# Optimization experiments

Hardware: AMD Instinct MI355X
Metric: run time of the kernel (lower is better)

## Reference

```python
import jax, jax.numpy as jnp
import numpy as np


def setup_inputs() -> dict:
    key = jax.random.key(0)
    kq, kk, kv = jax.random.split(key, 3)
    B, T, D = 8, 4096, 64
    q = jax.random.normal(kq, (B, T, D), dtype=jnp.float32)
    k = jax.random.normal(kk, (B, T, D), dtype=jnp.float32)
    v = jax.random.normal(kv, (B, T, D), dtype=jnp.float32)
    return {"q": q, "k": k, "v": v}


def reference(q, k, v):
    # q,k,v: [b, t, d]
    b, t_q, d = q.shape
    t_k = k.shape[1]
    scale = 1.0 / jnp.sqrt(jnp.asarray(d, dtype=q.dtype))
    qk = jnp.einsum('bqd,bkd->bqk', q, k) * scale  # [b, t_q, t_k]
    # causal mask: positions t2 > t1 set to -inf (replaces the Python double-loop)
    causal_mask = jnp.arange(t_k)[None, :] > jnp.arange(t_q)[:, None]  # [t_q, t_k]
    qk = jnp.where(causal_mask[None, :, :], -jnp.inf, qk)
    attn = jax.nn.softmax(qk, axis=-1)
    return jnp.einsum('bqk,bkd->bqd', attn, v)
```

## Files before the change

### kernel.cpp

```cpp
#include <hip/hip_runtime.h>

namespace {

constexpr float QSC = 0.18033688f;

typedef short bf16x8 __attribute__((ext_vector_type(8)));
typedef float f32x4 __attribute__((ext_vector_type(4)));

typedef __attribute__((address_space(3))) unsigned int lds_u32;
typedef __attribute__((address_space(1))) const unsigned int gbl_u32;

__device__ inline float exp2x(float x) { return __builtin_amdgcn_exp2f(x); }

__device__ inline unsigned int pack2(float a, float b) {
  unsigned int ua = __builtin_bit_cast(unsigned int, a);
  unsigned int ub = __builtin_bit_cast(unsigned int, b);
  ua = (ua + 0x8000u) >> 16;
  ub = (ub + 0x8000u) & 0xFFFF0000u;
  return ua | ub;
}

__device__ inline void gl_lds16(const unsigned short* g, unsigned short* l) {
  __builtin_amdgcn_global_load_lds((gbl_u32*)g, (lds_u32*)l, 16, 0, 0);
}

__device__ inline bf16x8 ld16(const unsigned short* p) {
  uint4 u = *(const uint4*)p;
  return __builtin_bit_cast(bf16x8, u);
}

__device__ inline void pswap32(unsigned int& a, unsigned int& b) {
  asm volatile("v_permlane32_swap_b32 %0, %1" : "+v"(a), "+v"(b));
}
__device__ inline void pswap16(unsigned int& a, unsigned int& b) {
  asm volatile("v_permlane16_swap_b32 %0, %1" : "+v"(a), "+v"(b));
}

__global__ __launch_bounds__(256) void prep(const float* __restrict__ K,
                                            const float* __restrict__ V,
                                            unsigned short* __restrict__ Kbf,
                                            unsigned short* __restrict__ Vtb) {
  __shared__ float Vl[64 * 65];
  const int bid = blockIdx.x;
  const int b = bid >> 6, kt = bid & 63;
  const int tid = threadIdx.x;
  const float4* Ks4 = (const float4*)(K + ((size_t)b * 4096 + kt * 64) * 64);
  const float4* Vs4 = (const float4*)(V + ((size_t)b * 4096 + kt * 64) * 64);
  #pragma unroll
  for (int i = 0; i < 4; ++i) {
    int idx = tid + 256 * i;
    int row = idx >> 4, c4 = idx & 15;
    float4 t = Ks4[idx];
    *(uint2*)&Kbf[((size_t)b * 4096 + kt * 64 + row) * 64 + c4 * 4] =
        make_uint2(pack2(t.x, t.y), pack2(t.z, t.w));
    float4 tv = Vs4[idx];
    float* d = &Vl[row * 65 + c4 * 4];
    d[0] = tv.x; d[1] = tv.y; d[2] = tv.z; d[3] = tv.w;
  }
  __syncthreads();
  #pragma unroll
  for (int i = 0; i < 4; ++i) {
    int idx = tid + 256 * i;
    int dd = idx >> 4, kc = idx & 15;
    float a  = Vl[(kc * 4 + 0) * 65 + dd];
    float b2 = Vl[(kc * 4 + 1) * 65 + dd];
    float c  = Vl[(kc * 4 + 2) * 65 + dd];
    float e  = Vl[(kc * 4 + 3) * 65 + dd];
    *(uint2*)&Vtb[((size_t)b * 64 + dd) * 4096 + kt * 64 + kc * 4] =
        make_uint2(pack2(a, b2), pack2(c, e));
  }
}

template <int NS>
__launch_bounds__(256, 5)
__global__ void fa_mfma(const float* __restrict__ Q,
                        float* __restrict__ O,
                        const unsigned short* __restrict__ Kbf,
                        const unsigned short* __restrict__ Vtb,
                        float* __restrict__ Opart,
                        float* __restrict__ lsum) {
  __shared__ __align__(16) unsigned short smem[16384];

  const int bid = blockIdx.x;
  const int qt = 63 - bid / (8 * NS);
  const int b  = (bid / NS) & 7;
  const int s  = bid % NS;

  const int tid  = threadIdx.x;
  const int wg   = tid >> 6;
  const int lane = tid & 63;
  const int quad = lane >> 4;
  const int lc   = lane & 15;

  unsigned short* Kb0 = smem;
  unsigned short* Kb1 = smem + 4096;
  unsigned short* Vb0 = smem + 8192;
  unsigned short* Vb1 = smem + 12288;

  const unsigned short* Kt_g = Kbf + (size_t)b * 4096 * 64;
  const unsigned short* Vt_g = Vtb + (size_t)b * 64 * 4096;

  const int r0 = wg * 16 + (lane >> 3);
  const int c0 = (lane & 7) ^ (r0 & 7);

  const int ph0 = (quad ^ (lc & 7)) * 8;
  const int ph1 = ((4 + quad) ^ (lc & 7)) * 8;

  const size_t tile_off = ((size_t)b * 4096 + (size_t)qt * 64) * 64;
  const float* Qb = Q + tile_off;

  const int nIter = (qt >= s) ? ((qt - s) / NS + 1) : 0;

  {
    const int kt0 = (s <= qt) ? s : qt;
    gl_lds16(Kt_g + (size_t)(kt0 * 64 + r0) * 64 + c0 * 8, Kb0 + wg * 1024);
    gl_lds16(Kt_g + (size_t)(kt0 * 64 + r0 + 8) * 64 + c0 * 8, Kb0 + wg * 1024 + 512);
    gl_lds16(Vt_g + (size_t)r0 * 4096 + kt0 * 64 + c0 * 8, Vb0 + wg * 1024);
    gl_lds16(Vt_g + (size_t)(r0 + 8) * 4096 + kt0 * 64 + c0 * 8, Vb0 + wg * 1024 + 512);
  }

  bf16x8 qf[2];
  {
    const float* qrow = Qb + (wg * 16 + lc) * 64 + quad * 8;
    #pragma unroll
    for (int ks = 0; ks < 2; ++ks) {
      float4 x = *(const float4*)(qrow + ks * 32);
      float4 y = *(const float4*)(qrow + ks * 32 + 4);
      uint4 u = make_uint4(pack2(x.x * QSC, x.y * QSC), pack2(x.z * QSC, x.w * QSC),
                           pack2(y.x * QSC, y.y * QSC), pack2(y.z * QSC, y.w * QSC));
      qf[ks] = __builtin_bit_cast(bf16x8, u);
    }
  }

  float l_i = 0.0f;
  f32x4 o[4];
  #pragma unroll
  for (int nt = 0; nt < 4; ++nt) o[nt] = f32x4{0.f, 0.f, 0.f, 0.f};

  const int qrow = wg * 16 + lc;

  auto body = [&](const unsigned short* Kcur, const unsigned short* Vcur, bool diag) __attribute__((always_inline)) {
    f32x4 st[4];
    __builtin_amdgcn_s_setprio(1);
    #pragma unroll
    for (int t = 0; t < 4; ++t) {
      f32x4 c = {0.f, 0.f, 0.f, 0.f};
      c = __builtin_amdgcn_mfma_f32_16x16x32_bf16(ld16(&Kcur[(t * 16 + lc) * 64 + ph0]), qf[0], c, 0, 0, 0);
      c = __builtin_amdgcn_mfma_f32_16x16x32_bf16(ld16(&Kcur[(t * 16 + lc) * 64 + ph1]), qf[1], c, 0, 0, 0);
      st[t] = c;
    }
    __builtin_amdgcn_s_setprio(0);

    unsigned int pc[4][2];
    #pragma unroll
    for (int t = 0; t < 4; ++t) {
      float e[4];
      #pragma unroll
      for (int r = 0; r < 4; ++r) {
        float v = st[t][r];
        if (diag) {
          int key_l = 16 * t + quad * 4 + r;
          if (key_l > qrow) v = -1e30f;
        }
        e[r] = exp2x(v);
      }
      l_i += (e[0] + e[1]) + (e[2] + e[3]);
      pc[t][0] = pack2(e[0], e[1]);
      pc[t][1] = pack2(e[2], e[3]);
    }

    __builtin_amdgcn_s_setprio(1);
    #pragma unroll
    for (int ks = 0; ks < 2; ++ks) {
      unsigned int x0 = pc[2 * ks][0], y0 = pc[2 * ks + 1][0];
      unsigned int x1 = pc[2 * ks][1], y1 = pc[2 * ks + 1][1];
      pswap32(x0, y0); pswap16(x0, y0);
      pswap32(x1, y1); pswap16(x1, y1);
      bf16x8 a = __builtin_bit_cast(bf16x8, make_uint4(x0, x1, y0, y1));
      const int ph = ks ? ph1 : ph0;
      #pragma unroll
      for (int nt = 0; nt < 4; ++nt) {
        o[nt] = __builtin_amdgcn_mfma_f32_16x16x32_bf16(a, ld16(&Vcur[(nt * 16 + lc) * 64 + ph]), o[nt], 0, 0, 0);
      }
    }
    __builtin_amdgcn_s_setprio(0);
  };

  for (int i = 0; i + 1 < nIter; ++i) {
    const unsigned short* Kcur = (i & 1) ? Kb1 : Kb0;
    const unsigned short* Vcur = (i & 1) ? Vb1 : Vb0;
    unsigned short* Knxt = (i & 1) ? Kb0 : Kb1;
    unsigned short* Vnxt = (i & 1) ? Vb0 : Vb1;

    asm volatile("s_waitcnt vmcnt(0)" ::: "memory");
    __builtin_amdgcn_s_barrier();

    const int ktn = NS * (i + 1) + s;
    const unsigned short* gk = Kt_g + (size_t)(ktn * 64) * 64;
    gl_lds16(gk + (size_t)r0 * 64 + c0 * 8, Knxt + wg * 1024);
    gl_lds16(gk + (size_t)(r0 + 8) * 64 + c0 * 8, Knxt + wg * 1024 + 512);
    const unsigned short* gv = Vt_g + ktn * 64;
    gl_lds16(gv + (size_t)r0 * 4096 + c0 * 8, Vnxt + wg * 1024);
    gl_lds16(gv + (size_t)(r0 + 8) * 4096 + c0 * 8, Vnxt + wg * 1024 + 512);

    body(Kcur, Vcur, false);
  }

  if (nIter > 0) {
    const int il = nIter - 1;
    const unsigned short* Kcur = (il & 1) ? Kb1 : Kb0;
    const unsigned short* Vcur = (il & 1) ? Vb1 : Vb0;
    asm volatile("s_waitcnt vmcnt(0)" ::: "memory");
    __builtin_amdgcn_s_barrier();
    body(Kcur, Vcur, (NS * il + s) == qt);
  }

  l_i += __shfl_xor(l_i, 16);
  l_i += __shfl_xor(l_i, 32);

  if constexpr (NS == 1) {
    float linv = 1.0f / l_i;
    float lv[4];
    #pragma unroll
    for (int r = 0; r < 4; ++r) lv[r] = __shfl(linv, quad * 4 + r);
    float* Ob = O + tile_off;
    #pragma unroll
    for (int r = 0; r < 4; ++r) {
      int row = wg * 16 + quad * 4 + r;
      #pragma unroll
      for (int nt = 0; nt < 4; ++nt)
        Ob[row * 64 + nt * 16 + lc] = o[nt][r] * lv[r];
    }
  } else {
    float* Oslot = (s == 0) ? (O + tile_off)
                            : (Opart + (size_t)(s - 1) * 2097152 + tile_off);
    #pragma unroll
    for (int r = 0; r < 4; ++r) {
      int row = wg * 16 + quad * 4 + r;
      #pragma unroll
      for (int nt = 0; nt < 4; ++nt)
        Oslot[row * 64 + nt * 16 + lc] = o[nt][r];
    }
    if (quad == 0)
      lsum[s * 32768 + b * 4096 + qt * 64 + wg * 16 + lc] = l_i;
  }
}

template <int NS>
__global__ __launch_bounds__(256) void fa_merge(float* __restrict__ O,
                                               const float* __restrict__ Opart,
                                               const float* __restrict__ lsum) {
  const int f = (blockIdx.x * 256 + threadIdx.x) * 4;
  const int row = f >> 6;
  float l = lsum[row];
  float4 acc = *(const float4*)&O[f];
  #pragma unroll
  for (int s2 = 1; s2 < NS; ++s2) {
    l += lsum[s2 * 32768 + row];
    float4 p = *(const float4*)&Opart[(size_t)(s2 - 1) * 2097152 + f];
    acc.x += p.x; acc.y += p.y; acc.z += p.z; acc.w += p.w;
  }
  const float linv = 1.0f / l;
  acc.x *= linv; acc.y *= linv; acc.z *= linv; acc.w *= linv;
  *(float4*)&O[f] = acc;
}

}

extern "C" void kernel_launch(void* const* d_in, const int* in_sizes, int n_in,
                              void* d_out, int out_size, void* d_ws, size_t ws_size,
                              hipStream_t stream) {
  const float* q = (const float*)d_in[0];
  const float* k = (const float*)d_in[1];
  const float* v = (const float*)d_in[2];
  float* out = (float*)d_out;

  unsigned short* Kbf = (unsigned short*)d_ws;
  unsigned short* Vtb = Kbf + (size_t)8 * 4096 * 64;
  float* Opart = (float*)(Vtb + (size_t)8 * 4096 * 64);
  auto need = [&](int ns) {
    return (size_t)16 * 1024 * 1024 / 2 +
           (size_t)(ns - 1) * 2097152 * 4 +
           (size_t)ns * 32768 * 4;
  };

  prep<<<dim3(512), dim3(256), 0, stream>>>(k, v, Kbf, Vtb);

  if (ws_size >= need(4)) {
    float* lsum = Opart + (size_t)3 * 2097152;
    fa_mfma<4><<<dim3(2048), dim3(256), 0, stream>>>(q, out, Kbf, Vtb, Opart, lsum);
    fa_merge<4><<<dim3(2048), dim3(256), 0, stream>>>(out, Opart, lsum);
  } else if (ws_size >= need(2)) {
    float* lsum = Opart + (size_t)1 * 2097152;
    fa_mfma<2><<<dim3(1024), dim3(256), 0, stream>>>(q, out, Kbf, Vtb, Opart, lsum);
    fa_merge<2><<<dim3(2048), dim3(256), 0, stream>>>(out, Opart, lsum);
  } else {
    fa_mfma<1><<<dim3(512), dim3(256), 0, stream>>>(q, out, Kbf, Vtb, nullptr, nullptr);
  }
}
```

Baseline: 108.8 us.

## Split attention tile 2x2 across waves by query and key halves, reduce via LDS

Each wave now handles 32 queries against 32 keys of the 64-key tile instead of 16 queries against all 64 keys. K and V fragments are loaded into registers once and reused across two query subtiles, which cuts LDS reads per MFMA. Partial outputs and row sums from the two key-half waves are combined through shared memory at the end. The change also switches bf16 packing to the hardware v_cvt_pk_bf16_f32 instruction and lowers the occupancy hint from 5 to 4 waves to allow more registers. The cost is extra registers for the doubled accumulators, plus an LDS reduction and barrier in the epilogue.

New measurement: 109.8 us. No clear change (+0.9%).

```diff
diff --git a/kernel.cpp b/kernel.cpp
--- a/kernel.cpp
+++ b/kernel.cpp
@@ -18,6 +18,12 @@
   ua = (ua + 0x8000u) >> 16;
   ub = (ub + 0x8000u) & 0xFFFF0000u;
   return ua | ub;
+}
+
+__device__ inline unsigned int cvtpk(float a, float b) {
+  unsigned int r;
+  asm("v_cvt_pk_bf16_f32 %0, %1, %2" : "=v"(r) : "v"(a), "v"(b));
+  return r;
 }
 
 __device__ inline void gl_lds16(const unsigned short* g, unsigned short* l) {
@@ -72,7 +78,7 @@
 }
 
 template <int NS>
-__launch_bounds__(256, 5)
+__launch_bounds__(256, 4)
 __global__ void fa_mfma(const float* __restrict__ Q,
                         float* __restrict__ O,
                         const unsigned short* __restrict__ Kbf,
@@ -87,7 +93,9 @@
   const int s  = bid % NS;
 
   const int tid  = threadIdx.x;
-  const int wg   = tid >> 6;
+  const int w    = tid >> 6;
+  const int kh   = w & 1;
+  const int qh   = w >> 1;
   const int lane = tid & 63;
   const int quad = lane >> 4;
   const int lc   = lane & 15;
@@ -100,11 +108,12 @@
   const unsigned short* Kt_g = Kbf + (size_t)b * 4096 * 64;
   const unsigned short* Vt_g = Vtb + (size_t)b * 64 * 4096;
 
-  const int r0 = wg * 16 + (lane >> 3);
+  const int r0 = w * 16 + (lane >> 3);
   const int c0 = (lane & 7) ^ (r0 & 7);
 
   const int ph0 = (quad ^ (lc & 7)) * 8;
   const int ph1 = ((4 + quad) ^ (lc & 7)) * 8;
+  const int phv = ((kh * 4 + quad) ^ (lc & 7)) * 8;
 
   const size_t tile_off = ((size_t)b * 4096 + (size_t)qt * 64) * 64;
   const float* Qb = Q + tile_off;
@@ -113,75 +122,89 @@
 
   {
     const int kt0 = (s <= qt) ? s : qt;
-    gl_lds16(Kt_g + (size_t)(kt0 * 64 + r0) * 64 + c0 * 8, Kb0 + wg * 1024);
-    gl_lds16(Kt_g + (size_t)(kt0 * 64 + r0 + 8) * 64 + c0 * 8, Kb0 + wg * 1024 + 512);
-    gl_lds16(Vt_g + (size_t)r0 * 4096 + kt0 * 64 + c0 * 8, Vb0 + wg * 1024);
-    gl_lds16(Vt_g + (size_t)(r0 + 8) * 4096 + kt0 * 64 + c0 * 8, Vb0 + wg * 1024 + 512);
-  }
-
-  bf16x8 qf[2];
-  {
-    const float* qrow = Qb + (wg * 16 + lc) * 64 + quad * 8;
+    gl_lds16(Kt_g + (size_t)(kt0 * 64 + r0) * 64 + c0 * 8, Kb0 + w * 1024);
+    gl_lds16(Kt_g + (size_t)(kt0 * 64 + r0 + 8) * 64 + c0 * 8, Kb0 + w * 1024 + 512);
+    gl_lds16(Vt_g + (size_t)r0 * 4096 + kt0 * 64 + c0 * 8, Vb0 + w * 1024);
+    gl_lds16(Vt_g + (size_t)(r0 + 8) * 4096 + kt0 * 64 + c0 * 8, Vb0 + w * 1024 + 512);
+  }
+
+  bf16x8 qf[2][2];
+  #pragma unroll
+  for (int tq = 0; tq < 2; ++tq) {
+    const float* qrow = Qb + (qh * 32 + tq * 16 + lc) * 64 + quad * 8;
     #pragma unroll
     for (int ks = 0; ks < 2; ++ks) {
       float4 x = *(const float4*)(qrow + ks * 32);
       float4 y = *(const float4*)(qrow + ks * 32 + 4);
       uint4 u = make_uint4(pack2(x.x * QSC, x.y * QSC), pack2(x.z * QSC, x.w * QSC),
                            pack2(y.x * QSC, y.y * QSC), pack2(y.z * QSC, y.w * QSC));
-      qf[ks] = __builtin_bit_cast(bf16x8, u);
-    }
-  }
-
-  float l_i = 0.0f;
-  f32x4 o[4];
-  #pragma unroll
-  for (int nt = 0; nt < 4; ++nt) o[nt] = f32x4{0.f, 0.f, 0.f, 0.f};
-
-  const int qrow = wg * 16 + lc;
+      qf[tq][ks] = __builtin_bit_cast(bf16x8, u);
+    }
+  }
+
+  float l4[2] = {0.0f, 0.0f};
+  f32x4 o[2][4];
+  #pragma unroll
+  for (int tq = 0; tq < 2; ++tq)
+    #pragma unroll
+    for (int td = 0; td < 4; ++td) o[tq][td] = f32x4{0.f, 0.f, 0.f, 0.f};
 
   auto body = [&](const unsigned short* Kcur, const unsigned short* Vcur, bool diag) __attribute__((always_inline)) {
-    f32x4 st[4];
+    bf16x8 kf[2][2];
+    #pragma unroll
+    for (int tk = 0; tk < 2; ++tk) {
+      kf[tk][0] = ld16(&Kcur[(kh * 32 + tk * 16 + lc) * 64 + ph0]);
+      kf[tk][1] = ld16(&Kcur[(kh * 32 + tk * 16 + lc) * 64 + ph1]);
+    }
+    f32x4 st[2][2];
     __builtin_amdgcn_s_setprio(1);
     #pragma unroll
-    for (int t = 0; t < 4; ++t) {
-      f32x4 c = {0.f, 0.f, 0.f, 0.f};
-      c = __builtin_amdgcn_mfma_f32_16x16x32_bf16(ld16(&Kcur[(t * 16 + lc) * 64 + ph0]), qf[0], c, 0, 0, 0);
-      c = __builtin_amdgcn_mfma_f32_16x16x32_bf16(ld16(&Kcur[(t * 16 + lc) * 64 + ph1]), qf[1], c, 0, 0, 0);
-      st[t] = c;
-    }
+    for (int tk = 0; tk < 2; ++tk)
+      #pragma unroll
+      for (int tq = 0; tq < 2; ++tq) {
+        f32x4 c = {0.f, 0.f, 0.f, 0.f};
+        c = __builtin_amdgcn_mfma_f32_16x16x32_bf16(kf[tk][0], qf[tq][0], c, 0, 0, 0);
+        c = __builtin_amdgcn_mfma_f32_16x16x32_bf16(kf[tk][1], qf[tq][1], c, 0, 0, 0);
+        st[tk][tq] = c;
+      }
     __builtin_amdgcn_s_setprio(0);
 
-    unsigned int pc[4][2];
-    #pragma unroll
-    for (int t = 0; t < 4; ++t) {
-      float e[4];
-      #pragma unroll
-      for (int r = 0; r < 4; ++r) {
-        float v = st[t][r];
-        if (diag) {
-          int key_l = 16 * t + quad * 4 + r;
-          if (key_l > qrow) v = -1e30f;
+    unsigned int pc[2][2][2];
+    #pragma unroll
+    for (int tk = 0; tk < 2; ++tk)
+      #pragma unroll
+      for (int tq = 0; tq < 2; ++tq) {
+        float e[4];
+        #pragma unroll
+        for (int r = 0; r < 4; ++r) {
+          float v = st[tk][tq][r];
+          if (diag) {
+            int key_l = kh * 32 + tk * 16 + quad * 4 + r;
+            int q_l   = qh * 32 + tq * 16 + lc;
+            if (key_l > q_l) v = -1e30f;
+          }
+          e[r] = exp2x(v);
         }
-        e[r] = exp2x(v);
-      }
-      l_i += (e[0] + e[1]) + (e[2] + e[3]);
-      pc[t][0] = pack2(e[0], e[1]);
-      pc[t][1] = pack2(e[2], e[3]);
-    }
-
+        l4[tq] += (e[0] + e[1]) + (e[2] + e[3]);
+        pc[tk][tq][0] = cvtpk(e[0], e[1]);
+        pc[tk][tq][1] = cvtpk(e[2], e[3]);
+      }
+
+    bf16x8 vf[4];
+    #pragma unroll
+    for (int td = 0; td < 4; ++td)
+      vf[td] = ld16(&Vcur[(td * 16 + lc) * 64 + phv]);
     __builtin_amdgcn_s_setprio(1);
     #pragma unroll
-    for (int ks = 0; ks < 2; ++ks) {
-      unsigned int x0 = pc[2 * ks][0], y0 = pc[2 * ks + 1][0];
-      unsigned int x1 = pc[2 * ks][1], y1 = pc[2 * ks + 1][1];
+    for (int tq = 0; tq < 2; ++tq) {
+      unsigned int x0 = pc[0][tq][0], y0 = pc[1][tq][0];
+      unsigned int x1 = pc[0][tq][1], y1 = pc[1][tq][1];
       pswap32(x0, y0); pswap16(x0, y0);
       pswap32(x1, y1); pswap16(x1, y1);
       bf16x8 a = __builtin_bit_cast(bf16x8, make_uint4(x0, x1, y0, y1));
-      const int ph = ks ? ph1 : ph0;
-      #pragma unroll
-      for (int nt = 0; nt < 4; ++nt) {
-        o[nt] = __builtin_amdgcn_mfma_f32_16x16x32_bf16(a, ld16(&Vcur[(nt * 16 + lc) * 64 + ph]), o[nt], 0, 0, 0);
-      }
+      #pragma unroll
+      for (int td = 0; td < 4; ++td)
+        o[tq][td] = __builtin_amdgcn_mfma_f32_16x16x32_bf16(a, vf[td], o[tq][td], 0, 0, 0);
     }
     __builtin_amdgcn_s_setprio(0);
   };
@@ -197,11 +220,11 @@
 
     const int ktn = NS * (i + 1) + s;
     const unsigned short* gk = Kt_g + (size_t)(ktn * 64) * 64;
-    gl_lds16(gk + (size_t)r0 * 64 + c0 * 8, Knxt + wg * 1024);
-    gl_lds16(gk + (size_t)(r0 + 8) * 64 + c0 * 8, Knxt + wg * 1024 + 512);
+    gl_lds16(gk + (size_t)r0 * 64 + c0 * 8, Knxt + w * 1024);
+    gl_lds16(gk + (size_t)(r0 + 8) * 64 + c0 * 8, Knxt + w * 1024 + 512);
     const unsigned short* gv = Vt_g + ktn * 64;
-    gl_lds16(gv + (size_t)r0 * 4096 + c0 * 8, Vnxt + wg * 1024);
-    gl_lds16(gv + (size_t)(r0 + 8) * 4096 + c0 * 8, Vnxt + wg * 1024 + 512);
+    gl_lds16(gv + (size_t)r0 * 4096 + c0 * 8, Vnxt + w * 1024);
+    gl_lds16(gv + (size_t)(r0 + 8) * 4096 + c0 * 8, Vnxt + w * 1024 + 512);
 
     body(Kcur, Vcur, false);
   }
@@ -215,34 +238,78 @@
     body(Kcur, Vcur, (NS * il + s) == qt);
   }
 
-  l_i += __shfl_xor(l_i, 16);
-  l_i += __shfl_xor(l_i, 32);
-
-  if constexpr (NS == 1) {
-    float linv = 1.0f / l_i;
-    float lv[4];
-    #pragma unroll
-    for (int r = 0; r < 4; ++r) lv[r] = __shfl(linv, quad * 4 + r);
-    float* Ob = O + tile_off;
-    #pragma unroll
-    for (int r = 0; r < 4; ++r) {
-      int row = wg * 16 + quad * 4 + r;
-      #pragma unroll
-      for (int nt = 0; nt < 4; ++nt)
-        Ob[row * 64 + nt * 16 + lc] = o[nt][r] * lv[r];
-    }
-  } else {
-    float* Oslot = (s == 0) ? (O + tile_off)
-                            : (Opart + (size_t)(s - 1) * 2097152 + tile_off);
-    #pragma unroll
-    for (int r = 0; r < 4; ++r) {
-      int row = wg * 16 + quad * 4 + r;
-      #pragma unroll
-      for (int nt = 0; nt < 4; ++nt)
-        Oslot[row * 64 + nt * 16 + lc] = o[nt][r];
-    }
-    if (quad == 0)
-      lsum[s * 32768 + b * 4096 + qt * 64 + wg * 16 + lc] = l_i;
+  __syncthreads();
+
+  #pragma unroll
+  for (int tq = 0; tq < 2; ++tq) {
+    l4[tq] += __shfl_xor(l4[tq], 16);
+    l4[tq] += __shfl_xor(l4[tq], 32);
+  }
+
+  constexpr int MS = 66;
+  float* buf  = (float*)smem;
+  float* lbuf = buf + 64 * MS;
+  if (kh == 1) {
+    #pragma unroll
+    for (int tq = 0; tq < 2; ++tq) {
+      #pragma unroll
+      for (int r = 0; r < 4; ++r) {
+        int row = qh * 32 + tq * 16 + quad * 4 + r;
+        #pragma unroll
+        for (int td = 0; td < 4; ++td)
+          buf[row * MS + td * 16 + lc] = o[tq][td][r];
+      }
+      if (quad == 0) lbuf[qh * 32 + tq * 16 + lc] = l4[tq];
+    }
+  }
+  __syncthreads();
+  if (kh == 0) {
+    #pragma unroll
+    for (int tq = 0; tq < 2; ++tq) {
+      l4[tq] += lbuf[qh * 32 + tq * 16 + lc];
+      #pragma unroll
+      for (int r = 0; r < 4; ++r) {
+        int row = qh * 32 + tq * 16 + quad * 4 + r;
+        #pragma unroll
+        for (int td = 0; td < 4; ++td)
+          o[tq][td][r] += buf[row * MS + td * 16 + lc];
+      }
+    }
+
+    if constexpr (NS == 1) {
+      float lv[2][4];
+      #pragma unroll
+      for (int tq = 0; tq < 2; ++tq) {
+        float linv = 1.0f / l4[tq];
+        #pragma unroll
+        for (int r = 0; r < 4; ++r) lv[tq][r] = __shfl(linv, quad * 4 + r);
+      }
+      float* Ob = O + tile_off;
+      #pragma unroll
+      for (int tq = 0; tq < 2; ++tq)
+        #pragma unroll
+        for (int r = 0; r < 4; ++r) {
+          int row = qh * 32 + tq * 16 + quad * 4 + r;
+          #pragma unroll
+          for (int td = 0; td < 4; ++td)
+            Ob[row * 64 + td * 16 + lc] = o[tq][td][r] * lv[tq][r];
+        }
+    } else {
+      float* Oslot = (s == 0) ? (O + tile_off)
+                              : (Opart + (size_t)(s - 1) * 2097152 + tile_off);
+      #pragma unroll
+      for (int tq = 0; tq < 2; ++tq) {
+        #pragma unroll
+        for (int r = 0; r < 4; ++r) {
+          int row = qh * 32 + tq * 16 + quad * 4 + r;
+          #pragma unroll
+          for (int td = 0; td < 4; ++td)
+            Oslot[row * 64 + td * 16 + lc] = o[tq][td][r];
+        }
+        if (quad == 0)
+          lsum[s * 32768 + b * 4096 + qt * 64 + qh * 32 + tq * 16 + lc] = l4[tq];
+      }
+    }
   }
 }
 
```

## Split key tile across wave pairs in 512-thread blocks, drop 4-way split

Applied to the files above, without the earlier changes.

Doubles the block to 8 waves. Each pair of waves shares 16 query rows and splits the 64-key tile in half, and the two partial results are reduced through LDS at the end. The 4-way key split is removed in favour of the 2-way path, and block-index mapping in prep, main and merge is reordered to interleave batches. A hardware bf16 pack instruction replaces the manual rounding. This aims to raise in-block parallelism and cut the partial-sum workspace traffic, at the cost of an extra LDS reduction, a barrier, and fewer concurrent key splits per tile.

After: 108.4 us. About the same (-0.4%).

```diff
diff --git a/kernel.cpp b/kernel.cpp
--- a/kernel.cpp
+++ b/kernel.cpp
@@ -20,6 +20,12 @@
   return ua | ub;
 }
 
+__device__ inline unsigned int cvtpk(float a, float b) {
+  unsigned int r;
+  asm("v_cvt_pk_bf16_f32 %0, %1, %2" : "=v"(r) : "v"(a), "v"(b));
+  return r;
+}
+
 __device__ inline void gl_lds16(const unsigned short* g, unsigned short* l) {
   __builtin_amdgcn_global_load_lds((gbl_u32*)g, (lds_u32*)l, 16, 0, 0);
 }
@@ -42,7 +48,7 @@
                                             unsigned short* __restrict__ Vtb) {
   __shared__ float Vl[64 * 65];
   const int bid = blockIdx.x;
-  const int b = bid >> 6, kt = bid & 63;
+  const int b = bid & 7, kt = bid >> 3;
   const int tid = threadIdx.x;
   const float4* Ks4 = (const float4*)(K + ((size_t)b * 4096 + kt * 64) * 64);
   const float4* Vs4 = (const float4*)(V + ((size_t)b * 4096 + kt * 64) * 64);
@@ -72,7 +78,7 @@
 }
 
 template <int NS>
-__launch_bounds__(256, 5)
+__launch_bounds__(512, 8)
 __global__ void fa_mfma(const float* __restrict__ Q,
                         float* __restrict__ O,
                         const unsigned short* __restrict__ Kbf,
@@ -82,12 +88,14 @@
   __shared__ __align__(16) unsigned short smem[16384];
 
   const int bid = blockIdx.x;
-  const int qt = 63 - bid / (8 * NS);
-  const int b  = (bid / NS) & 7;
-  const int s  = bid % NS;
+  int b, qt, s;
+  if constexpr (NS == 2) { qt = 63 - (bid >> 4); b = bid & 7; s = (bid >> 3) & 1; }
+  else                   { qt = 63 - (bid >> 3); b = bid & 7; s = 0; }
 
   const int tid  = threadIdx.x;
-  const int wg   = tid >> 6;
+  const int w    = tid >> 6;
+  const int kh   = w & 1;
+  const int qh   = w >> 1;
   const int lane = tid & 63;
   const int quad = lane >> 4;
   const int lc   = lane & 15;
@@ -100,11 +108,12 @@
   const unsigned short* Kt_g = Kbf + (size_t)b * 4096 * 64;
   const unsigned short* Vt_g = Vtb + (size_t)b * 64 * 4096;
 
-  const int r0 = wg * 16 + (lane >> 3);
+  const int r0 = w * 8 + (lane >> 3);
   const int c0 = (lane & 7) ^ (r0 & 7);
 
   const int ph0 = (quad ^ (lc & 7)) * 8;
   const int ph1 = ((4 + quad) ^ (lc & 7)) * 8;
+  const int phv = ((kh * 4 + quad) ^ (lc & 7)) * 8;
 
   const size_t tile_off = ((size_t)b * 4096 + (size_t)qt * 64) * 64;
   const float* Qb = Q + tile_off;
@@ -113,15 +122,13 @@
 
   {
     const int kt0 = (s <= qt) ? s : qt;
-    gl_lds16(Kt_g + (size_t)(kt0 * 64 + r0) * 64 + c0 * 8, Kb0 + wg * 1024);
-    gl_lds16(Kt_g + (size_t)(kt0 * 64 + r0 + 8) * 64 + c0 * 8, Kb0 + wg * 1024 + 512);
-    gl_lds16(Vt_g + (size_t)r0 * 4096 + kt0 * 64 + c0 * 8, Vb0 + wg * 1024);
-    gl_lds16(Vt_g + (size_t)(r0 + 8) * 4096 + kt0 * 64 + c0 * 8, Vb0 + wg * 1024 + 512);
+    gl_lds16(Kt_g + (size_t)(kt0 * 64 + r0) * 64 + c0 * 8, Kb0 + w * 512);
+    gl_lds16(Vt_g + (size_t)r0 * 4096 + kt0 * 64 + c0 * 8, Vb0 + w * 512);
   }
 
   bf16x8 qf[2];
   {
-    const float* qrow = Qb + (wg * 16 + lc) * 64 + quad * 8;
+    const float* qrow = Qb + (qh * 16 + lc) * 64 + quad * 8;
     #pragma unroll
     for (int ks = 0; ks < 2; ++ks) {
       float4 x = *(const float4*)(qrow + ks * 32);
@@ -135,53 +142,60 @@
   float l_i = 0.0f;
   f32x4 o[4];
   #pragma unroll
-  for (int nt = 0; nt < 4; ++nt) o[nt] = f32x4{0.f, 0.f, 0.f, 0.f};
-
-  const int qrow = wg * 16 + lc;
+  for (int td = 0; td < 4; ++td) o[td] = f32x4{0.f, 0.f, 0.f, 0.f};
+
+  const int q_l = qh * 16 + lc;
 
   auto body = [&](const unsigned short* Kcur, const unsigned short* Vcur, bool diag) __attribute__((always_inline)) {
-    f32x4 st[4];
+    bf16x8 kf[2][2];
+    #pragma unroll
+    for (int tk = 0; tk < 2; ++tk) {
+      kf[tk][0] = ld16(&Kcur[(kh * 32 + tk * 16 + lc) * 64 + ph0]);
+      kf[tk][1] = ld16(&Kcur[(kh * 32 + tk * 16 + lc) * 64 + ph1]);
+    }
+    f32x4 st[2];
     __builtin_amdgcn_s_setprio(1);
     #pragma unroll
-    for (int t = 0; t < 4; ++t) {
+    for (int tk = 0; tk < 2; ++tk) {
       f32x4 c = {0.f, 0.f, 0.f, 0.f};
-      c = __builtin_amdgcn_mfma_f32_16x16x32_bf16(ld16(&Kcur[(t * 16 + lc) * 64 + ph0]), qf[0], c, 0, 0, 0);
-      c = __builtin_amdgcn_mfma_f32_16x16x32_bf16(ld16(&Kcur[(t * 16 + lc) * 64 + ph1]), qf[1], c, 0, 0, 0);
-      st[t] = c;
+      c = __builtin_amdgcn_mfma_f32_16x16x32_bf16(kf[tk][0], qf[0], c, 0, 0, 0);
+      c = __builtin_amdgcn_mfma_f32_16x16x32_bf16(kf[tk][1], qf[1], c, 0, 0, 0);
+      st[tk] = c;
     }
     __builtin_amdgcn_s_setprio(0);
 
-    unsigned int pc[4][2];
-    #pragma unroll
-    for (int t = 0; t < 4; ++t) {
+    unsigned int pc[2][2];
+    #pragma unroll
+    for (int tk = 0; tk < 2; ++tk) {
       float e[4];
       #pragma unroll
       for (int r = 0; r < 4; ++r) {
-        float v = st[t][r];
+        float v = st[tk][r];
         if (diag) {
-          int key_l = 16 * t + quad * 4 + r;
-          if (key_l > qrow) v = -1e30f;
+          int key_l = kh * 32 + tk * 16 + quad * 4 + r;
+          if (key_l > q_l) v = -1e30f;
         }
         e[r] = exp2x(v);
       }
       l_i += (e[0] + e[1]) + (e[2] + e[3]);
-      pc[t][0] = pack2(e[0], e[1]);
-      pc[t][1] = pack2(e[2], e[3]);
-    }
-
+      pc[tk][0] = cvtpk(e[0], e[1]);
+      pc[tk][1] = cvtpk(e[2], e[3]);
+    }
+
+    bf16x8 vf[4];
+    #pragma unroll
+    for (int td = 0; td < 4; ++td)
+      vf[td] = ld16(&Vcur[(td * 16 + lc) * 64 + phv]);
     __builtin_amdgcn_s_setprio(1);
-    #pragma unroll
-    for (int ks = 0; ks < 2; ++ks) {
-      unsigned int x0 = pc[2 * ks][0], y0 = pc[2 * ks + 1][0];
-      unsigned int x1 = pc[2 * ks][1], y1 = pc[2 * ks + 1][1];
+    {
+      unsigned int x0 = pc[0][0], y0 = pc[1][0];
+      unsigned int x1 = pc[0][1], y1 = pc[1][1];
       pswap32(x0, y0); pswap16(x0, y0);
       pswap32(x1, y1); pswap16(x1, y1);
       bf16x8 a = __builtin_bit_cast(bf16x8, make_uint4(x0, x1, y0, y1));
-      const int ph = ks ? ph1 : ph0;
-      #pragma unroll
-      for (int nt = 0; nt < 4; ++nt) {
-        o[nt] = __builtin_amdgcn_mfma_f32_16x16x32_bf16(a, ld16(&Vcur[(nt * 16 + lc) * 64 + ph]), o[nt], 0, 0, 0);
-      }
+      #pragma unroll
+      for (int td = 0; td < 4; ++td)
+        o[td] = __builtin_amdgcn_mfma_f32_16x16x32_bf16(a, vf[td], o[td], 0, 0, 0);
     }
     __builtin_amdgcn_s_setprio(0);
   };
@@ -196,12 +210,8 @@
     __builtin_amdgcn_s_barrier();
 
     const int ktn = NS * (i + 1) + s;
-    const unsigned short* gk = Kt_g + (size_t)(ktn * 64) * 64;
-    gl_lds16(gk + (size_t)r0 * 64 + c0 * 8, Knxt + wg * 1024);
-    gl_lds16(gk + (size_t)(r0 + 8) * 64 + c0 * 8, Knxt + wg * 1024 + 512);
-    const unsigned short* gv = Vt_g + ktn * 64;
-    gl_lds16(gv + (size_t)r0 * 4096 + c0 * 8, Vnxt + wg * 1024);
-    gl_lds16(gv + (size_t)(r0 + 8) * 4096 + c0 * 8, Vnxt + wg * 1024 + 512);
+    gl_lds16(Kt_g + (size_t)(ktn * 64 + r0) * 64 + c0 * 8, Knxt + w * 512);
+    gl_lds16(Vt_g + (size_t)r0 * 4096 + ktn * 64 + c0 * 8, Vnxt + w * 512);
 
     body(Kcur, Vcur, false);
   }
@@ -215,34 +225,60 @@
     body(Kcur, Vcur, (NS * il + s) == qt);
   }
 
+  __syncthreads();
+
   l_i += __shfl_xor(l_i, 16);
   l_i += __shfl_xor(l_i, 32);
 
-  if constexpr (NS == 1) {
-    float linv = 1.0f / l_i;
-    float lv[4];
-    #pragma unroll
-    for (int r = 0; r < 4; ++r) lv[r] = __shfl(linv, quad * 4 + r);
-    float* Ob = O + tile_off;
+  constexpr int MS = 66;
+  float* buf  = (float*)smem;
+  float* lbuf = buf + 64 * MS;
+  if (kh == 1) {
     #pragma unroll
     for (int r = 0; r < 4; ++r) {
-      int row = wg * 16 + quad * 4 + r;
-      #pragma unroll
-      for (int nt = 0; nt < 4; ++nt)
-        Ob[row * 64 + nt * 16 + lc] = o[nt][r] * lv[r];
-    }
-  } else {
-    float* Oslot = (s == 0) ? (O + tile_off)
-                            : (Opart + (size_t)(s - 1) * 2097152 + tile_off);
+      int row = qh * 16 + quad * 4 + r;
+      #pragma unroll
+      for (int td = 0; td < 4; ++td)
+        buf[row * MS + td * 16 + lc] = o[td][r];
+    }
+    if (quad == 0) lbuf[qh * 16 + lc] = l_i;
+  }
+  __syncthreads();
+  if (kh == 0) {
+    l_i += lbuf[qh * 16 + lc];
     #pragma unroll
     for (int r = 0; r < 4; ++r) {
-      int row = wg * 16 + quad * 4 + r;
-      #pragma unroll
-      for (int nt = 0; nt < 4; ++nt)
-        Oslot[row * 64 + nt * 16 + lc] = o[nt][r];
-    }
-    if (quad == 0)
-      lsum[s * 32768 + b * 4096 + qt * 64 + wg * 16 + lc] = l_i;
+      int row = qh * 16 + quad * 4 + r;
+      #pragma unroll
+      for (int td = 0; td < 4; ++td)
+        o[td][r] += buf[row * MS + td * 16 + lc];
+    }
+
+    if constexpr (NS == 1) {
+      float linv = 1.0f / l_i;
+      float lv[4];
+      #pragma unroll
+      for (int r = 0; r < 4; ++r) lv[r] = __shfl(linv, quad * 4 + r);
+      float* Ob = O + tile_off;
+      #pragma unroll
+      for (int r = 0; r < 4; ++r) {
+        int row = qh * 16 + quad * 4 + r;
+        #pragma unroll
+        for (int td = 0; td < 4; ++td)
+          Ob[row * 64 + td * 16 + lc] = o[td][r] * lv[r];
+      }
+    } else {
+      float* Oslot = (s == 0) ? (O + tile_off) : (Opart + tile_off);
+      #pragma unroll
+      for (int r = 0; r < 4; ++r) {
+        int row = qh * 16 + quad * 4 + r;
+        #pragma unroll
+        for (int td = 0; td < 4; ++td)
+          Oslot[row * 64 + td * 16 + lc] = o[td][r];
+      }
+      if (quad == 0)
+        lsum[s * 32768 + b * 4096 + qt * 64 + qh * 16 + lc] = l_i;
+    }
   }
 }
 
@@ -250,7 +286,9 @@
 __global__ __launch_bounds__(256) void fa_merge(float* __restrict__ O,
                                                const float* __restrict__ Opart,
                                                const float* __restrict__ lsum) {
-  const int f = (blockIdx.x * 256 + threadIdx.x) * 4;
+  const int b = blockIdx.x & 7;
+  const int c = blockIdx.x >> 3;
+  const int f = b * 262144 + c * 1024 + threadIdx.x * 4;
   const int row = f >> 6;
   float l = lsum[row];
   float4 acc = *(const float4*)&O[f];
@@ -286,15 +324,11 @@
 
   prep<<<dim3(512), dim3(256), 0, stream>>>(k, v, Kbf, Vtb);
 
-  if (ws_size >= need(4)) {
-    float* lsum = Opart + (size_t)3 * 2097152;
-    fa_mfma<4><<<dim3(2048), dim3(256), 0, stream>>>(q, out, Kbf, Vtb, Opart, lsum);
-    fa_merge<4><<<dim3(2048), dim3(256), 0, stream>>>(out, Opart, lsum);
-  } else if (ws_size >= need(2)) {
+  if (ws_size >= need(2)) {
     float* lsum = Opart + (size_t)1 * 2097152;
-    fa_mfma<2><<<dim3(1024), dim3(256), 0, stream>>>(q, out, Kbf, Vtb, Opart, lsum);
+    fa_mfma<2><<<dim3(1024), dim3(512), 0, stream>>>(q, out, Kbf, Vtb, Opart, lsum);
     fa_merge<2><<<dim3(2048), dim3(256), 0, stream>>>(out, Opart, lsum);
   } else {
-    fa_mfma<1><<<dim3(512), dim3(256), 0, stream>>>(q, out, Kbf, Vtb, nullptr, nullptr);
-  }
-}
+    fa_mfma<1><<<dim3(512), dim3(512), 0, stream>>>(q, out, Kbf, Vtb, nullptr, nullptr);
+  }
+}
```
